# Optimization experiments

Measured on AMD Instinct MI355X. Metric: run time of the kernel, lower is better.

## Reference

```python
import jax, jax.numpy as jnp
import numpy as np

HIDDEN_DIM = 2048
PROJ_IN = 3 * 56 * 56  # 9408
PROJ_OUT = 1024
N_CLASSES = 65
BS = 2048


def setup_inputs() -> dict:
    key = jax.random.key(0)
    k1, k2, k3, k4, k5, k6 = jax.random.split(key, 6)
    z1 = jax.random.normal(k1, (BS, HIDDEN_DIM), dtype=jnp.float32)
    z2 = jax.random.normal(k2, (BS, 3, 56, 56), dtype=jnp.float32)
    # nn.Linear params: weight [out, in], bias [out]
    W_proj = jax.random.normal(k3, (PROJ_OUT, PROJ_IN), dtype=jnp.float32) * (PROJ_IN ** -0.5)
    b_proj = jax.random.normal(k4, (PROJ_OUT,), dtype=jnp.float32) * 0.01
    W_fc = jax.random.normal(k5, (N_CLASSES, HIDDEN_DIM + PROJ_OUT), dtype=jnp.float32) * ((HIDDEN_DIM + PROJ_OUT) ** -0.5)
    b_fc = jax.random.normal(k6, (N_CLASSES,), dtype=jnp.float32) * 0.01
    return {"z1": z1, "z2": z2, "W_proj": W_proj, "b_proj": b_proj, "W_fc": W_fc, "b_fc": b_fc}


def reference(z1, z2, W_proj, b_proj, W_fc, b_fc):
    bs = z1.shape[0]
    # z2 branch: flatten -> Linear -> ReLU -> detach (stop_gradient)
    z2f = z2.reshape(bs, -1)                                  # [bs, 9408]
    z2p = jax.nn.relu(z2f @ W_proj.T + b_proj)                # [bs, 1024]
    z2p = jax.lax.stop_gradient(z2p)
    # test=True path. fc_c2(cat(z1_i, z2_j)) = z1_i @ W1^T + z2_j @ W2^T + b
    # (exact split of the linear layer; same math as repeat+cat+linear).
    d1 = z1.shape[1]
    s1 = z1 @ W_fc[:, :d1].T                                  # [bs, 65]
    s2 = z2p @ W_fc[:, d1:].T                                 # [bs, 65]
    pair = s1[:, None, :] + s2[None, :, :] + b_fc             # [bs, bs, 65]
    return jnp.sum(pair, axis=1)                              # [bs, 65]
```

## Files before the change

kernel.cpp:

```cpp
#include <hip/hip_runtime.h>
#include <hip/hip_bf16.h>
#include <stdint.h>

#define BSZ   2048
#define KDIM  9408
#define NPROJ 1024
#define D1    2048
#define NCLS  65
#define NPAD  80
#define DFC   3072
#define KSTEPS 147

using bf16x8 = __attribute__((ext_vector_type(8))) short;
using f32x4  = __attribute__((ext_vector_type(4))) float;

__device__ __forceinline__ short f2bf(float f) {
    __hip_bfloat16 h = __float2bfloat16(f);
    return __builtin_bit_cast(short, h);
}

__device__ __forceinline__ void gload16(const void* g, void* l) {
    __builtin_amdgcn_global_load_lds(
        (const __attribute__((address_space(1))) void*)g,
        (__attribute__((address_space(3))) void*)l, 16, 0, 0);
}

__global__ void cvt_bf16(const float* __restrict__ src, short* __restrict__ dst, int n8)
{
    int i = blockIdx.x * blockDim.x + threadIdx.x;
    const int stride = gridDim.x * blockDim.x;
    for (; i < n8; i += stride) {
        const float4 v0 = *(const float4*)(src + (size_t)i * 8);
        const float4 v1 = *(const float4*)(src + (size_t)i * 8 + 4);
        bf16x8 s;
        s[0] = f2bf(v0.x); s[1] = f2bf(v0.y); s[2] = f2bf(v0.z); s[3] = f2bf(v0.w);
        s[4] = f2bf(v1.x); s[5] = f2bf(v1.y); s[6] = f2bf(v1.z); s[7] = f2bf(v1.w);
        *(bf16x8*)(dst + (size_t)i * 8) = s;
    }
}

__global__ void w1pad_kernel(const float* __restrict__ Wf, short* __restrict__ W1)
{
    const int chunk = blockIdx.x * 256 + threadIdx.x;
    const int row = chunk >> 8;
    const int col = (chunk & 255) * 8;
    bf16x8 s;
    if (row < NCLS) {
        const float* g = Wf + (size_t)row * DFC + col;
        float4 v0 = *(const float4*)g;
        float4 v1 = *(const float4*)(g + 4);
        s[0] = f2bf(v0.x); s[1] = f2bf(v0.y); s[2] = f2bf(v0.z); s[3] = f2bf(v0.w);
        s[4] = f2bf(v1.x); s[5] = f2bf(v1.y); s[6] = f2bf(v1.z); s[7] = f2bf(v1.w);
    } else {
        s = (bf16x8){0,0,0,0,0,0,0,0};
    }
    *(bf16x8*)(W1 + (size_t)row * D1 + col) = s;
}

template<int KS>
__global__ __launch_bounds__(256, 2)
void gemm_bf16(const short* __restrict__ A,
               const short* __restrict__ B,
               float* __restrict__ Cpart)
{
    __shared__ __align__(16) short Alds[128 * 64];
    __shared__ __align__(16) short Blds[128 * 64];

    const int t = threadIdx.x;
    const int cpx = (128 * KS) >> 3;
    int bid = blockIdx.x;
    bid = (bid & 7) * cpx + (bid >> 3);
    const int bm = bid & 15;
    const int bn = (bid >> 4) & 7;
    const int ks = bid >> 7;
    const int nsteps = KSTEPS / KS;

    const int l = t & 63, w = t >> 6;
    const int wr = w >> 1, wc = w & 1;
    const int lr = l & 15, lg = l >> 4;

    const int srow = t >> 3;
    const int scol = (t & 7) * 8;

    const short* ga = A + (size_t)(bm * 128) * KDIM;
    const short* gb = B + (size_t)(bn * 128) * KDIM;

    f32x4 acc[4][4];
#pragma unroll
    for (int m = 0; m < 4; ++m)
#pragma unroll
        for (int n = 0; n < 4; ++n)
            acc[m][n] = (f32x4){0.f, 0.f, 0.f, 0.f};

    for (int step = 0; step < nsteps; ++step) {
        const int k0 = (ks * nsteps + step) * 64;

#pragma unroll
        for (int p = 0; p < 4; ++p)
            gload16(ga + (size_t)(p * 32 + srow) * KDIM + k0 + scol,
                    (char*)Alds + p * 4096 + t * 16);
#pragma unroll
        for (int p = 0; p < 4; ++p)
            gload16(gb + (size_t)(p * 32 + srow) * KDIM + k0 + scol,
                    (char*)Blds + p * 4096 + t * 16);
        __syncthreads();

#pragma unroll
        for (int kk = 0; kk < 2; ++kk) {
            const int kb = kk * 32 + lg * 8;
            bf16x8 af[4], bfr[4];
#pragma unroll
            for (int m = 0; m < 4; ++m)
                af[m] = *(bf16x8*)&Alds[(wr * 64 + m * 16 + lr) * 64 + kb];
#pragma unroll
            for (int n = 0; n < 4; ++n)
                bfr[n] = *(bf16x8*)&Blds[(wc * 64 + n * 16 + lr) * 64 + kb];
#pragma unroll
            for (int m = 0; m < 4; ++m)
#pragma unroll
                for (int n = 0; n < 4; ++n)
                    acc[m][n] = __builtin_amdgcn_mfma_f32_16x16x32_bf16(
                        af[m], bfr[n], acc[m][n], 0, 0, 0);
        }
        __syncthreads();
    }

    float* Cp = Cpart + ((size_t)ks * BSZ + bm * 128) * NPROJ + bn * 128;
#pragma unroll
    for (int m = 0; m < 4; ++m)
#pragma unroll
        for (int r = 0; r < 4; ++r) {
            const int i = wr * 64 + m * 16 + lg * 4 + r;
#pragma unroll
            for (int n = 0; n < 4; ++n)
                Cp[(size_t)i * NPROJ + wc * 64 + n * 16 + lr] = acc[m][n][r];
        }
}

template<int KS2>
__global__ __launch_bounds__(256, 2)
void fc2_gemm(const float* __restrict__ z1,
              const short* __restrict__ W1,
              float* __restrict__ Cp2)
{
    __shared__ __align__(16) short Alds[128 * 64];
    __shared__ __align__(16) short Blds[NPAD * 64];

    const int t  = threadIdx.x;
    const int bm = blockIdx.x & 15;
    const int ks = blockIdx.x >> 4;
    const int nsteps = (D1 / 64) / KS2;

    const int l = t & 63, w = t >> 6;
    const int lr = l & 15, lg = l >> 4;
    const int srow = t >> 3;
    const int scol = (t & 7) * 8;

    f32x4 acc[2][5];
#pragma unroll
    for (int m = 0; m < 2; ++m)
#pragma unroll
        for (int n = 0; n < 5; ++n)
            acc[m][n] = (f32x4){0.f, 0.f, 0.f, 0.f};

    for (int step = 0; step < nsteps; ++step) {
        const int k0 = (ks * nsteps + step) * 64;

#pragma unroll
        for (int p = 0; p < 4; ++p) {
            const int row = p * 32 + srow;
            const float* g = z1 + (size_t)(bm * 128 + row) * D1 + k0 + scol;
            float4 v0 = *(const float4*)g;
            float4 v1 = *(const float4*)(g + 4);
            bf16x8 s;
            s[0] = f2bf(v0.x); s[1] = f2bf(v0.y); s[2] = f2bf(v0.z); s[3] = f2bf(v0.w);
            s[4] = f2bf(v1.x); s[5] = f2bf(v1.y); s[6] = f2bf(v1.z); s[7] = f2bf(v1.w);
            *(bf16x8*)&Alds[row * 64 + scol] = s;
        }
#pragma unroll
        for (int p = 0; p < 2; ++p) {
            const int chunk = p * 256 + t;
            gload16(W1 + (size_t)(chunk >> 3) * D1 + k0 + (chunk & 7) * 8,
                    (char*)Blds + chunk * 16);
        }
        if (t < 128) {
            const int chunk = 512 + t;
            gload16(W1 + (size_t)(chunk >> 3) * D1 + k0 + (chunk & 7) * 8,
                    (char*)Blds + chunk * 16);
        }
        __syncthreads();

#pragma unroll
        for (int kk = 0; kk < 2; ++kk) {
            const int kb = kk * 32 + lg * 8;
            bf16x8 af[2], bfr[5];
#pragma unroll
            for (int m = 0; m < 2; ++m)
                af[m] = *(bf16x8*)&Alds[(w * 32 + m * 16 + lr) * 64 + kb];
#pragma unroll
            for (int n = 0; n < 5; ++n)
                bfr[n] = *(bf16x8*)&Blds[(n * 16 + lr) * 64 + kb];
#pragma unroll
            for (int m = 0; m < 2; ++m)
#pragma unroll
                for (int n = 0; n < 5; ++n)
                    acc[m][n] = __builtin_amdgcn_mfma_f32_16x16x32_bf16(
                        af[m], bfr[n], acc[m][n], 0, 0, 0);
        }
        __syncthreads();
    }

    float* C = Cp2 + ((size_t)ks * BSZ + bm * 128) * NPAD;
#pragma unroll
    for (int m = 0; m < 2; ++m)
#pragma unroll
        for (int r = 0; r < 4; ++r) {
            const int i = w * 32 + m * 16 + lg * 4 + r;
#pragma unroll
            for (int n = 0; n < 5; ++n)
                C[(size_t)i * NPAD + n * 16 + lr] = acc[m][n][r];
        }
}

template<int KS2>
__global__ void reduce2_kernel(const float* __restrict__ Cp2,
                               const float* __restrict__ sconst,
                               float* __restrict__ out)
{
    const int i = blockIdx.x * 2 + (threadIdx.x >> 7);
    const int c = threadIdx.x & 127;
    if (c >= NCLS) return;
    float s = 0.f;
#pragma unroll
    for (int ksi = 0; ksi < KS2; ++ksi)
        s += Cp2[((size_t)ksi * BSZ + i) * NPAD + c];
    out[(size_t)i * NCLS + c] = 2048.0f * s + sconst[c];
}

template<int KS>
__global__ __launch_bounds__(256, 2)
void gemm_relu_f32(const float* __restrict__ A, const float* __restrict__ B,
                   const float* __restrict__ bias, float* __restrict__ Cpart,
                   float* __restrict__ colsum)
{
    __shared__ __align__(16) short Alds[128 * 64];
    __shared__ __align__(16) short Blds[128 * 64];

    const int t  = threadIdx.x;
    const int bm = blockIdx.x, bn = blockIdx.y, ks = blockIdx.z;
    const int nsteps = KSTEPS / KS;
    const int l  = t & 63, w = t >> 6;
    const int wr = w >> 1, wc = w & 1;
    const int lr = l & 15, lg = l >> 4;
    const int srow = t >> 3, scol = (t & 7) * 8;
    const int sswz = (srow & 7) * 8;
    const int rswz = (lr & 7) * 8;

    const float* ga = A + (size_t)(bm * 128 + srow) * KDIM + scol;
    const float* gb = B + (size_t)(bn * 128 + srow) * KDIM + scol;

    f32x4 acc[4][4];
#pragma unroll
    for (int m = 0; m < 4; ++m)
#pragma unroll
        for (int n = 0; n < 4; ++n)
            acc[m][n] = (f32x4){0.f, 0.f, 0.f, 0.f};

    for (int step = 0; step < nsteps; ++step) {
        const int k0 = (ks * nsteps + step) * 64;
#pragma unroll
        for (int p = 0; p < 4; ++p) {
            const float* g = ga + (size_t)(p * 32) * KDIM + k0;
            float4 v0 = *(const float4*)g;
            float4 v1 = *(const float4*)(g + 4);
            bf16x8 s;
            s[0] = f2bf(v0.x); s[1] = f2bf(v0.y); s[2] = f2bf(v0.z); s[3] = f2bf(v0.w);
            s[4] = f2bf(v1.x); s[5] = f2bf(v1.y); s[6] = f2bf(v1.z); s[7] = f2bf(v1.w);
            *(bf16x8*)&Alds[(p * 32 + srow) * 64 + (scol ^ sswz)] = s;
        }
#pragma unroll
        for (int p = 0; p < 4; ++p) {
            const float* g = gb + (size_t)(p * 32) * KDIM + k0;
            float4 v0 = *(const float4*)g;
            float4 v1 = *(const float4*)(g + 4);
            bf16x8 s;
            s[0] = f2bf(v0.x); s[1] = f2bf(v0.y); s[2] = f2bf(v0.z); s[3] = f2bf(v0.w);
            s[4] = f2bf(v1.x); s[5] = f2bf(v1.y); s[6] = f2bf(v1.z); s[7] = f2bf(v1.w);
            *(bf16x8*)&Blds[(p * 32 + srow) * 64 + (scol ^ sswz)] = s;
        }
        __syncthreads();
#pragma unroll
        for (int kk = 0; kk < 2; ++kk) {
            const int kb = (kk * 32 + lg * 8) ^ rswz;
            bf16x8 af[4], bfr[4];
#pragma unroll
            for (int m = 0; m < 4; ++m)
                af[m] = *(bf16x8*)&Alds[(wr * 64 + m * 16 + lr) * 64 + kb];
#pragma unroll
            for (int n = 0; n < 4; ++n)
                bfr[n] = *(bf16x8*)&Blds[(wc * 64 + n * 16 + lr) * 64 + kb];
#pragma unroll
            for (int m = 0; m < 4; ++m)
#pragma unroll
                for (int n = 0; n < 4; ++n)
                    acc[m][n] = __builtin_amdgcn_mfma_f32_16x16x32_bf16(
                        af[m], bfr[n], acc[m][n], 0, 0, 0);
        }
        __syncthreads();
    }

    if constexpr (KS == 1) {
        __shared__ float cls[128];
        if (t < 128) cls[t] = 0.f;
        __syncthreads();
#pragma unroll
        for (int n = 0; n < 4; ++n) {
            const int o = wc * 64 + n * 16 + lr;
            const float bv = bias[bn * 128 + o];
            float ps = 0.f;
#pragma unroll
            for (int m = 0; m < 4; ++m)
#pragma unroll
                for (int r = 0; r < 4; ++r) {
                    float v = acc[m][n][r] + bv;
                    ps += v > 0.f ? v : 0.f;
                }
            atomicAdd(&cls[o], ps);
        }
        __syncthreads();
        if (t < 128) atomicAdd(&colsum[bn * 128 + t], cls[t]);
    } else {
        float* Cp = Cpart + ((size_t)ks * BSZ + bm * 128) * NPROJ + bn * 128;
#pragma unroll
        for (int m = 0; m < 4; ++m)
#pragma unroll
            for (int r = 0; r < 4; ++r) {
                const int i = wr * 64 + m * 16 + lg * 4 + r;
#pragma unroll
                for (int n = 0; n < 4; ++n)
                    Cp[(size_t)i * NPROJ + wc * 64 + n * 16 + lr] = acc[m][n][r];
            }
    }
}

template<int KS>
__global__ void reduce_colsum(const float* __restrict__ Cpart,
                              const float* __restrict__ bias,
                              float* __restrict__ colsum)
{
    const int col = blockIdx.y * 256 + threadIdx.x;
    const int r0  = blockIdx.x * 16;
    const float bv = bias[col];
    float p = 0.f;
    for (int r = 0; r < 16; ++r) {
        float s = bv;
#pragma unroll
        for (int si = 0; si < KS; ++si)
            s += Cpart[((size_t)si * BSZ + r0 + r) * NPROJ + col];
        p += fmaxf(s, 0.f);
    }
    atomicAdd(&colsum[col], p);
}

__global__ void sconst_kernel(const float* __restrict__ colsum,
                              const float* __restrict__ Wfc,
                              const float* __restrict__ bfc,
                              float* __restrict__ sconst)
{
    const int c = blockIdx.x;
    const int l = threadIdx.x;
    const float* wr = Wfc + (size_t)c * DFC + D1;
    float p = 0.f;
#pragma unroll
    for (int j = 0; j < 16; ++j)
        p += colsum[l + j * 64] * wr[l + j * 64];
#pragma unroll
    for (int off = 32; off; off >>= 1)
        p += __shfl_xor(p, off);
    if (l == 0) sconst[c] = p + 2048.0f * bfc[c];
}

__global__ __launch_bounds__(256)
void fc1_kernel(const float* __restrict__ z1,
                const float* __restrict__ Wfc,
                const float* __restrict__ sconst,
                float* __restrict__ out)
{
    const int l = threadIdx.x & 63;
    const int w = threadIdx.x >> 6;
    const int i = blockIdx.x * 4 + w;
    const float* zr = z1 + (size_t)i * D1;
    float4 za[8];
#pragma unroll
    for (int j = 0; j < 8; ++j)
        za[j] = *(const float4*)&zr[j * 256 + l * 4];
    for (int c = 0; c < NCLS; ++c) {
        const float* wrow = Wfc + (size_t)c * DFC;
        float acc = 0.f;
#pragma unroll
        for (int j = 0; j < 8; ++j) {
            float4 wv = *(const float4*)&wrow[j * 256 + l * 4];
            acc += za[j].x * wv.x + za[j].y * wv.y + za[j].z * wv.z + za[j].w * wv.w;
        }
#pragma unroll
        for (int off = 32; off; off >>= 1)
            acc += __shfl_xor(acc, off);
        if (l == 0) out[(size_t)i * NCLS + c] = 2048.0f * acc + sconst[c];
    }
}

extern "C" void kernel_launch(void* const* d_in, const int* in_sizes, int n_in,
                              void* d_out, int out_size, void* d_ws, size_t ws_size,
                              hipStream_t stream)
{
    (void)in_sizes; (void)n_in; (void)out_size;
    const float* z1  = (const float*)d_in[0];
    const float* z2  = (const float*)d_in[1];
    const float* Wp  = (const float*)d_in[2];
    const float* bp  = (const float*)d_in[3];
    const float* Wf  = (const float*)d_in[4];
    const float* bfc = (const float*)d_in[5];
    float* out = (float*)d_out;

    float* colsum = (float*)d_ws;
    float* sconst = (float*)d_ws + 1024;
    size_t off = 8192;

    const size_t w1_sz = (size_t)NPAD * D1 * 2;
    const size_t c2_sz = (size_t)16 * BSZ * NPAD * 4;
    const bool fc2_ok = ws_size >= off + w1_sz + c2_sz;
    short* W1  = (short*)((char*)d_ws + off);
    float* Cp2 = (float*)((char*)d_ws + off + w1_sz);
    if (fc2_ok) off += w1_sz + c2_sz;

    const size_t z2bf_sz = (size_t)BSZ * KDIM * 2;
    const size_t wp_sz   = (size_t)NPROJ * KDIM * 2;
    const size_t perKS   = (size_t)BSZ * NPROJ * 4;
    const size_t rem = ws_size > off ? ws_size - off : 0;

    hipMemsetAsync(d_ws, 0, 8192, stream);

    int main_ks = 0;
    if      (rem >= z2bf_sz + wp_sz + 7 * perKS) main_ks = 7;
    else if (rem >= z2bf_sz + wp_sz + 3 * perKS) main_ks = 3;
    else if (rem >= z2bf_sz + wp_sz + 1 * perKS) main_ks = 1;

    if (main_ks > 0) {
        short* z2bf  = (short*)((char*)d_ws + off);
        short* wpbf  = (short*)((char*)d_ws + off + z2bf_sz);
        float* Cpart = (float*)((char*)d_ws + off + z2bf_sz + wp_sz);
        cvt_bf16<<<2048, 256, 0, stream>>>(z2, z2bf, BSZ * KDIM / 8);
        cvt_bf16<<<1024, 256, 0, stream>>>(Wp, wpbf, NPROJ * KDIM / 8);
        if (main_ks == 7) {
            gemm_bf16<7><<<896, 256, 0, stream>>>(z2bf, wpbf, Cpart);
            reduce_colsum<7><<<dim3(128, 4), 256, 0, stream>>>(Cpart, bp, colsum);
        } else if (main_ks == 3) {
            gemm_bf16<3><<<384, 256, 0, stream>>>(z2bf, wpbf, Cpart);
            reduce_colsum<3><<<dim3(128, 4), 256, 0, stream>>>(Cpart, bp, colsum);
        } else {
            gemm_bf16<1><<<128, 256, 0, stream>>>(z2bf, wpbf, Cpart);
            reduce_colsum<1><<<dim3(128, 4), 256, 0, stream>>>(Cpart, bp, colsum);
        }
    } else if (rem >= 7 * perKS) {
        float* Cpart = (float*)((char*)d_ws + off);
        gemm_relu_f32<7><<<dim3(16, 8, 7), 256, 0, stream>>>(z2, Wp, bp, Cpart, colsum);
        reduce_colsum<7><<<dim3(128, 4), 256, 0, stream>>>(Cpart, bp, colsum);
    } else {
        gemm_relu_f32<1><<<dim3(16, 8, 1), 256, 0, stream>>>(z2, Wp, bp,
                                                             (float*)((char*)d_ws + off), colsum);
    }

    sconst_kernel<<<65, 64, 0, stream>>>(colsum, Wf, bfc, sconst);

    if (fc2_ok) {
        w1pad_kernel<<<80, 256, 0, stream>>>(Wf, W1);
        fc2_gemm<16><<<256, 256, 0, stream>>>(z1, W1, Cp2);
        reduce2_kernel<16><<<1024, 256, 0, stream>>>(Cp2, sconst, out);
    } else {
        fc1_kernel<<<512, 256, 0, stream>>>(z1, Wf, sconst, out);
    }
}
```

Measured before the change: 249.4 us.

## Fuse conversions and memset, co-launch fc2 GEMM with projection GEMM

Merges the z2, W_proj and W_fc bf16 conversions and the workspace zeroing into one fused_cvt launch. It then runs the projection GEMM and the fc2 GEMM as separate block ranges of a single combined kernel, with launch bounds raised to 4 blocks per CU. This removes several launches and lets the small fc2 work fill idle CU slots next to the big GEMM. The higher occupancy target may squeeze registers, and the fc2 blocks compete with the main GEMM for bandwidth.

```diff
diff --git a/kernel.cpp b/kernel.cpp
--- a/kernel.cpp
+++ b/kernel.cpp
@@ -25,18 +25,252 @@
         (__attribute__((address_space(3))) void*)l, 16, 0, 0);
 }
 
+__device__ __forceinline__ bf16x8 cvt8(const float* g) {
+    float4 v0 = *(const float4*)g;
+    float4 v1 = *(const float4*)(g + 4);
+    bf16x8 s;
+    s[0] = f2bf(v0.x); s[1] = f2bf(v0.y); s[2] = f2bf(v0.z); s[3] = f2bf(v0.w);
+    s[4] = f2bf(v1.x); s[5] = f2bf(v1.y); s[6] = f2bf(v1.z); s[7] = f2bf(v1.w);
+    return s;
+}
+
+#define NC_Z2 (BSZ * KDIM / 8)
+#define NC_WP (NPROJ * KDIM / 8)
+#define NC_W1 (NPAD * D1 / 8)
+#define NC_TOT (NC_Z2 + NC_WP + NC_W1)
+
+__global__ void fused_cvt(const float* __restrict__ z2, short* __restrict__ z2bf,
+                          const float* __restrict__ Wp, short* __restrict__ wpbf,
+                          const float* __restrict__ Wf, short* __restrict__ W1,
+                          float* __restrict__ wshead)
+{
+    const int gid = blockIdx.x * blockDim.x + threadIdx.x;
+    if (gid < 2048) wshead[gid] = 0.f;
+    const int stride = gridDim.x * blockDim.x;
+    for (int i = gid; i < NC_TOT; i += stride) {
+        if (i < NC_Z2) {
+            *(bf16x8*)(z2bf + (size_t)i * 8) = cvt8(z2 + (size_t)i * 8);
+        } else if (i < NC_Z2 + NC_WP) {
+            const int j = i - NC_Z2;
+            *(bf16x8*)(wpbf + (size_t)j * 8) = cvt8(Wp + (size_t)j * 8);
+        } else {
+            const int c = i - NC_Z2 - NC_WP;
+            const int row = c >> 8;
+            const int col = (c & 255) * 8;
+            bf16x8 s = (bf16x8){0,0,0,0,0,0,0,0};
+            if (row < NCLS) s = cvt8(Wf + (size_t)row * DFC + col);
+            *(bf16x8*)(W1 + (size_t)row * D1 + col) = s;
+        }
+    }
+}
+
+template<int KS>
+__global__ __launch_bounds__(256, 4)
+void gemm_combo(const short* __restrict__ A,
+                const short* __restrict__ B,
+                float* __restrict__ Cpart,
+                const float* __restrict__ z1,
+                const short* __restrict__ W1,
+                float* __restrict__ Cp2)
+{
+    __shared__ __align__(16) char smem[32768];
+    short* Alds = (short*)smem;
+    short* Blds = (short*)(smem + 16384);
+
+    const int t = threadIdx.x;
+    const int l = t & 63, w = t >> 6;
+    const int lr = l & 15, lg = l >> 4;
+    const int srow = t >> 3;
+    const int scol = (t & 7) * 8;
+
+    if (blockIdx.x < 128 * KS) {
+        const int cpx = (128 * KS) >> 3;
+        int bid = blockIdx.x;
+        bid = (bid & 7) * cpx + (bid >> 3);
+        const int bm = bid & 15;
+        const int bn = (bid >> 4) & 7;
+        const int ks = bid >> 7;
+        const int nsteps = KSTEPS / KS;
+
+        const int wr = w >> 1, wc = w & 1;
+        const short* ga = A + (size_t)(bm * 128) * KDIM;
+        const short* gb = B + (size_t)(bn * 128) * KDIM;
+
+        f32x4 acc[4][4];
+#pragma unroll
+        for (int m = 0; m < 4; ++m)
+#pragma unroll
+            for (int n = 0; n < 4; ++n)
+                acc[m][n] = (f32x4){0.f, 0.f, 0.f, 0.f};
+
+        for (int step = 0; step < nsteps; ++step) {
+            const int k0 = (ks * nsteps + step) * 64;
+#pragma unroll
+            for (int p = 0; p < 4; ++p)
+                gload16(ga + (size_t)(p * 32 + srow) * KDIM + k0 + scol,
+                        (char*)Alds + p * 4096 + t * 16);
+#pragma unroll
+            for (int p = 0; p < 4; ++p)
+                gload16(gb + (size_t)(p * 32 + srow) * KDIM + k0 + scol,
+                        (char*)Blds + p * 4096 + t * 16);
+            __syncthreads();
+
+#pragma unroll
+            for (int kk = 0; kk < 2; ++kk) {
+                const int kb = kk * 32 + lg * 8;
+                bf16x8 af[4], bfr[4];
+#pragma unroll
+                for (int m = 0; m < 4; ++m)
+                    af[m] = *(bf16x8*)&Alds[(wr * 64 + m * 16 + lr) * 64 + kb];
+#pragma unroll
+                for (int n = 0; n < 4; ++n)
+                    bfr[n] = *(bf16x8*)&Blds[(wc * 64 + n * 16 + lr) * 64 + kb];
+#pragma unroll
+                for (int m = 0; m < 4; ++m)
+#pragma unroll
+                    for (int n = 0; n < 4; ++n)
+                        acc[m][n] = __builtin_amdgcn_mfma_f32_16x16x32_bf16(
+                            af[m], bfr[n], acc[m][n], 0, 0, 0);
+            }
+            __syncthreads();
+        }
+
+        float* Cp = Cpart + ((size_t)ks * BSZ + bm * 128) * NPROJ + bn * 128;
+#pragma unroll
+        for (int m = 0; m < 4; ++m)
+#pragma unroll
+            for (int r = 0; r < 4; ++r) {
+                const int i = wr * 64 + m * 16 + lg * 4 + r;
+#pragma unroll
+                for (int n = 0; n < 4; ++n)
+                    Cp[(size_t)i * NPROJ + wc * 64 + n * 16 + lr] = acc[m][n][r];
+            }
+    } else {
+        const int fbid = blockIdx.x - 128 * KS;
+        const int bm = fbid & 15;
+        const int ks = fbid >> 4;
+
+        f32x4 acc[2][5];
+#pragma unroll
+        for (int m = 0; m < 2; ++m)
+#pragma unroll
+            for (int n = 0; n < 5; ++n)
+                acc[m][n] = (f32x4){0.f, 0.f, 0.f, 0.f};
+
+#pragma unroll
+        for (int step = 0; step < 2; ++step) {
+            const int k0 = (ks * 2 + step) * 64;
+
+#pragma unroll
+            for (int p = 0; p < 4; ++p) {
+                const int row = p * 32 + srow;
+                *(bf16x8*)&Alds[row * 64 + scol] =
+                    cvt8(z1 + (size_t)(bm * 128 + row) * D1 + k0 + scol);
+            }
+#pragma unroll
+            for (int p = 0; p < 2; ++p) {
+                const int chunk = p * 256 + t;
+                gload16(W1 + (size_t)(chunk >> 3) * D1 + k0 + (chunk & 7) * 8,
+                        (char*)Blds + chunk * 16);
+            }
+            if (t < 128) {
+                const int chunk = 512 + t;
+                gload16(W1 + (size_t)(chunk >> 3) * D1 + k0 + (chunk & 7) * 8,
+                        (char*)Blds + chunk * 16);
+            }
+            __syncthreads();
+
+#pragma unroll
+            for (int kk = 0; kk < 2; ++kk) {
+                const int kb = kk * 32 + lg * 8;
+                bf16x8 af[2], bfr[5];
+#pragma unroll
+                for (int m = 0; m < 2; ++m)
+                    af[m] = *(bf16x8*)&Alds[(w * 32 + m * 16 + lr) * 64 + kb];
+#pragma unroll
+                for (int n = 0; n < 5; ++n)
+                    bfr[n] = *(bf16x8*)&Blds[(n * 16 + lr) * 64 + kb];
+#pragma unroll
+                for (int m = 0; m < 2; ++m)
+#pragma unroll
+                    for (int n = 0; n < 5; ++n)
+                        acc[m][n] = __builtin_amdgcn_mfma_f32_16x16x32_bf16(
+                            af[m], bfr[n], acc[m][n], 0, 0, 0);
+            }
+            __syncthreads();
+        }
+
+        float* C = Cp2 + ((size_t)ks * BSZ + bm * 128) * NPAD;
+#pragma unroll
+        for (int m = 0; m < 2; ++m)
+#pragma unroll
+            for (int r = 0; r < 4; ++r) {
+                const int i = w * 32 + m * 16 + lg * 4 + r;
+#pragma unroll
+                for (int n = 0; n < 5; ++n)
+                    C[(size_t)i * NPAD + n * 16 + lr] = acc[m][n][r];
+            }
+    }
+}
+
+template<int KS>
+__global__ void reduce_colsum(const float* __restrict__ Cpart,
+                              const float* __restrict__ bias,
+                              float* __restrict__ colsum)
+{
+    const int col = blockIdx.y * 256 + threadIdx.x;
+    const int r0  = blockIdx.x * 16;
+    const float bv = bias[col];
+    float p = 0.f;
+    for (int r = 0; r < 16; ++r) {
+        float s = bv;
+#pragma unroll
+        for (int si = 0; si < KS; ++si)
+            s += Cpart[((size_t)si * BSZ + r0 + r) * NPROJ + col];
+        p += fmaxf(s, 0.f);
+    }
+    atomicAdd(&colsum[col], p);
+}
+
+__global__ void sconst_kernel(const float* __restrict__ colsum,
+                              const float* __restrict__ Wfc,
+                              const float* __restrict__ bfc,
+                              float* __restrict__ sconst)
+{
+    const int c = blockIdx.x;
+    const int l = threadIdx.x;
+    const float* wr = Wfc + (size_t)c * DFC + D1;
+    float p = 0.f;
+#pragma unroll
+    for (int j = 0; j < 16; ++j)
+        p += colsum[l + j * 64] * wr[l + j * 64];
+#pragma unroll
+    for (int off = 32; off; off >>= 1)
+        p += __shfl_xor(p, off);
+    if (l == 0) sconst[c] = p + 2048.0f * bfc[c];
+}
+
+template<int KS2>
+__global__ void reduce2_kernel(const float* __restrict__ Cp2,
+                               const float* __restrict__ sconst,
+                               float* __restrict__ out)
+{
+    const int i = blockIdx.x * 2 + (threadIdx.x >> 7);
+    const int c = threadIdx.x & 127;
+    if (c >= NCLS) return;
+    float s = 0.f;
+#pragma unroll
+    for (int ksi = 0; ksi < KS2; ++ksi)
+        s += Cp2[((size_t)ksi * BSZ + i) * NPAD + c];
+    out[(size_t)i * NCLS + c] = 2048.0f * s + sconst[c];
+}
+
 __global__ void cvt_bf16(const float* __restrict__ src, short* __restrict__ dst, int n8)
 {
     int i = blockIdx.x * blockDim.x + threadIdx.x;
     const int stride = gridDim.x * blockDim.x;
-    for (; i < n8; i += stride) {
-        const float4 v0 = *(const float4*)(src + (size_t)i * 8);
-        const float4 v1 = *(const float4*)(src + (size_t)i * 8 + 4);
-        bf16x8 s;
-        s[0] = f2bf(v0.x); s[1] = f2bf(v0.y); s[2] = f2bf(v0.z); s[3] = f2bf(v0.w);
-        s[4] = f2bf(v1.x); s[5] = f2bf(v1.y); s[6] = f2bf(v1.z); s[7] = f2bf(v1.w);
-        *(bf16x8*)(dst + (size_t)i * 8) = s;
-    }
+    for (; i < n8; i += stride)
+        *(bf16x8*)(dst + (size_t)i * 8) = cvt8(src + (size_t)i * 8);
 }
 
 __global__ void w1pad_kernel(const float* __restrict__ Wf, short* __restrict__ W1)
@@ -44,28 +278,18 @@
     const int chunk = blockIdx.x * 256 + threadIdx.x;
     const int row = chunk >> 8;
     const int col = (chunk & 255) * 8;
-    bf16x8 s;
-    if (row < NCLS) {
-        const float* g = Wf + (size_t)row * DFC + col;
-        float4 v0 = *(const float4*)g;
-        float4 v1 = *(const float4*)(g + 4);
-        s[0] = f2bf(v0.x); s[1] = f2bf(v0.y); s[2] = f2bf(v0.z); s[3] = f2bf(v0.w);
-        s[4] = f2bf(v1.x); s[5] = f2bf(v1.y); s[6] = f2bf(v1.z); s[7] = f2bf(v1.w);
-    } else {
-        s = (bf16x8){0,0,0,0,0,0,0,0};
-    }
+    bf16x8 s = (bf16x8){0,0,0,0,0,0,0,0};
+    if (row < NCLS) s = cvt8(Wf + (size_t)row * DFC + col);
     *(bf16x8*)(W1 + (size_t)row * D1 + col) = s;
 }
 
 template<int KS>
 __global__ __launch_bounds__(256, 2)
-void gemm_bf16(const short* __restrict__ A,
-               const short* __restrict__ B,
+void gemm_bf16(const short* __restrict__ A, const short* __restrict__ B,
                float* __restrict__ Cpart)
 {
     __shared__ __align__(16) short Alds[128 * 64];
     __shared__ __align__(16) short Blds[128 * 64];
-
     const int t = threadIdx.x;
     const int cpx = (128 * KS) >> 3;
     int bid = blockIdx.x;
@@ -74,27 +298,19 @@
     const int bn = (bid >> 4) & 7;
     const int ks = bid >> 7;
     const int nsteps = KSTEPS / KS;
-
     const int l = t & 63, w = t >> 6;
     const int wr = w >> 1, wc = w & 1;
     const int lr = l & 15, lg = l >> 4;
-
-    const int srow = t >> 3;
-    const int scol = (t & 7) * 8;
-
+    const int srow = t >> 3, scol = (t & 7) * 8;
     const short* ga = A + (size_t)(bm * 128) * KDIM;
     const short* gb = B + (size_t)(bn * 128) * KDIM;
-
     f32x4 acc[4][4];
 #pragma unroll
     for (int m = 0; m < 4; ++m)
 #pragma unroll
-        for (int n = 0; n < 4; ++n)
-            acc[m][n] = (f32x4){0.f, 0.f, 0.f, 0.f};
-
+        for (int n = 0; n < 4; ++n) acc[m][n] = (f32x4){0.f,0.f,0.f,0.f};
     for (int step = 0; step < nsteps; ++step) {
         const int k0 = (ks * nsteps + step) * 64;
-
 #pragma unroll
         for (int p = 0; p < 4; ++p)
             gload16(ga + (size_t)(p * 32 + srow) * KDIM + k0 + scol,
@@ -104,7 +320,6 @@
             gload16(gb + (size_t)(p * 32 + srow) * KDIM + k0 + scol,
                     (char*)Blds + p * 4096 + t * 16);
         __syncthreads();
-
 #pragma unroll
         for (int kk = 0; kk < 2; ++kk) {
             const int kb = kk * 32 + lg * 8;
@@ -124,7 +339,6 @@
         }
         __syncthreads();
     }
-
     float* Cp = Cpart + ((size_t)ks * BSZ + bm * 128) * NPROJ + bn * 128;
 #pragma unroll
     for (int m = 0; m < 4; ++m)
@@ -139,43 +353,30 @@
 
 template<int KS2>
 __global__ __launch_bounds__(256, 2)
-void fc2_gemm(const float* __restrict__ z1,
-              const short* __restrict__ W1,
+void fc2_gemm(const float* __restrict__ z1, const short* __restrict__ W1,
               float* __restrict__ Cp2)
 {
     __shared__ __align__(16) short Alds[128 * 64];
     __shared__ __align__(16) short Blds[NPAD * 64];
-
     const int t  = threadIdx.x;
     const int bm = blockIdx.x & 15;
     const int ks = blockIdx.x >> 4;
     const int nsteps = (D1 / 64) / KS2;
-
     const int l = t & 63, w = t >> 6;
     const int lr = l & 15, lg = l >> 4;
-    const int srow = t >> 3;
-    const int scol = (t & 7) * 8;
-
+    const int srow = t >> 3, scol = (t & 7) * 8;
     f32x4 acc[2][5];
 #pragma unroll
     for (int m = 0; m < 2; ++m)
 #pragma unroll
-        for (int n = 0; n < 5; ++n)
-            acc[m][n] = (f32x4){0.f, 0.f, 0.f, 0.f};
-
+        for (int n = 0; n < 5; ++n) acc[m][n] = (f32x4){0.f,0.f,0.f,0.f};
     for (int step = 0; step < nsteps; ++step) {
         const int k0 = (ks * nsteps + step) * 64;
-
 #pragma unroll
         for (int p = 0; p < 4; ++p) {
             const int row = p * 32 + srow;
-            const float* g = z1 + (size_t)(bm * 128 + row) * D1 + k0 + scol;
-            float4 v0 = *(const float4*)g;
-            float4 v1 = *(const float4*)(g + 4);
-            bf16x8 s;
-            s[0] = f2bf(v0.x); s[1] = f2bf(v0.y); s[2] = f2bf(v0.z); s[3] = f2bf(v0.w);
-            s[4] = f2bf(v1.x); s[5] = f2bf(v1.y); s[6] = f2bf(v1.z); s[7] = f2bf(v1.w);
-            *(bf16x8*)&Alds[row * 64 + scol] = s;
+            *(bf16x8*)&Alds[row * 64 + scol] =
+                cvt8(z1 + (size_t)(bm * 128 + row) * D1 + k0 + scol);
         }
 #pragma unroll
         for (int p = 0; p < 2; ++p) {
@@ -189,7 +390,6 @@
                     (char*)Blds + chunk * 16);
         }
         __syncthreads();
-
 #pragma unroll
         for (int kk = 0; kk < 2; ++kk) {
             const int kb = kk * 32 + lg * 8;
@@ -209,7 +409,6 @@
         }
         __syncthreads();
     }
-
     float* C = Cp2 + ((size_t)ks * BSZ + bm * 128) * NPAD;
 #pragma unroll
     for (int m = 0; m < 2; ++m)
@@ -220,21 +419,6 @@
             for (int n = 0; n < 5; ++n)
                 C[(size_t)i * NPAD + n * 16 + lr] = acc[m][n][r];
         }
-}
-
-template<int KS2>
-__global__ void reduce2_kernel(const float* __restrict__ Cp2,
-                               const float* __restrict__ sconst,
-                               float* __restrict__ out)
-{
-    const int i = blockIdx.x * 2 + (threadIdx.x >> 7);
-    const int c = threadIdx.x & 127;
-    if (c >= NCLS) return;
-    float s = 0.f;
-#pragma unroll
-    for (int ksi = 0; ksi < KS2; ++ksi)
-        s += Cp2[((size_t)ksi * BSZ + i) * NPAD + c];
-    out[(size_t)i * NCLS + c] = 2048.0f * s + sconst[c];
 }
 
 template<int KS>
@@ -245,7 +429,6 @@
 {
     __shared__ __align__(16) short Alds[128 * 64];
     __shared__ __align__(16) short Blds[128 * 64];
-
     const int t  = threadIdx.x;
     const int bm = blockIdx.x, bn = blockIdx.y, ks = blockIdx.z;
     const int nsteps = KSTEPS / KS;
@@ -255,39 +438,23 @@
     const int srow = t >> 3, scol = (t & 7) * 8;
     const int sswz = (srow & 7) * 8;
     const int rswz = (lr & 7) * 8;
-
     const float* ga = A + (size_t)(bm * 128 + srow) * KDIM + scol;
     const float* gb = B + (size_t)(bn * 128 + srow) * KDIM + scol;
-
     f32x4 acc[4][4];
 #pragma unroll
     for (int m = 0; m < 4; ++m)
 #pragma unroll
-        for (int n = 0; n < 4; ++n)
-            acc[m][n] = (f32x4){0.f, 0.f, 0.f, 0.f};
-
+        for (int n = 0; n < 4; ++n) acc[m][n] = (f32x4){0.f,0.f,0.f,0.f};
     for (int step = 0; step < nsteps; ++step) {
         const int k0 = (ks * nsteps + step) * 64;
 #pragma unroll
-        for (int p = 0; p < 4; ++p) {
-            const float* g = ga + (size_t)(p * 32) * KDIM + k0;
-            float4 v0 = *(const float4*)g;
-            float4 v1 = *(const float4*)(g + 4);
-            bf16x8 s;
-            s[0] = f2bf(v0.x); s[1] = f2bf(v0.y); s[2] = f2bf(v0.z); s[3] = f2bf(v0.w);
-            s[4] = f2bf(v1.x); s[5] = f2bf(v1.y); s[6] = f2bf(v1.z); s[7] = f2bf(v1.w);
-            *(bf16x8*)&Alds[(p * 32 + srow) * 64 + (scol ^ sswz)] = s;
-        }
-#pragma unroll
-        for (int p = 0; p < 4; ++p) {
-            const float* g = gb + (size_t)(p * 32) * KDIM + k0;
-            float4 v0 = *(const float4*)g;
-            float4 v1 = *(const float4*)(g + 4);
-            bf16x8 s;
-            s[0] = f2bf(v0.x); s[1] = f2bf(v0.y); s[2] = f2bf(v0.z); s[3] = f2bf(v0.w);
-            s[4] = f2bf(v1.x); s[5] = f2bf(v1.y); s[6] = f2bf(v1.z); s[7] = f2bf(v1.w);
-            *(bf16x8*)&Blds[(p * 32 + srow) * 64 + (scol ^ sswz)] = s;
-        }
+        for (int p = 0; p < 4; ++p)
+            *(bf16x8*)&Alds[(p * 32 + srow) * 64 + (scol ^ sswz)] =
+                cvt8(ga + (size_t)(p * 32) * KDIM + k0);
+#pragma unroll
+        for (int p = 0; p < 4; ++p)
+            *(bf16x8*)&Blds[(p * 32 + srow) * 64 + (scol ^ sswz)] =
+                cvt8(gb + (size_t)(p * 32) * KDIM + k0);
         __syncthreads();
 #pragma unroll
         for (int kk = 0; kk < 2; ++kk) {
@@ -308,7 +475,6 @@
         }
         __syncthreads();
     }
-
     if constexpr (KS == 1) {
         __shared__ float cls[128];
         if (t < 128) cls[t] = 0.f;
@@ -343,48 +509,9 @@
     }
 }
 
-template<int KS>
-__global__ void reduce_colsum(const float* __restrict__ Cpart,
-                              const float* __restrict__ bias,
-                              float* __restrict__ colsum)
-{
-    const int col = blockIdx.y * 256 + threadIdx.x;
-    const int r0  = blockIdx.x * 16;
-    const float bv = bias[col];
-    float p = 0.f;
-    for (int r = 0; r < 16; ++r) {
-        float s = bv;
-#pragma unroll
-        for (int si = 0; si < KS; ++si)
-            s += Cpart[((size_t)si * BSZ + r0 + r) * NPROJ + col];
-        p += fmaxf(s, 0.f);
-    }
-    atomicAdd(&colsum[col], p);
-}
-
-__global__ void sconst_kernel(const float* __restrict__ colsum,
-                              const float* __restrict__ Wfc,
-                              const float* __restrict__ bfc,
-                              float* __restrict__ sconst)
-{
-    const int c = blockIdx.x;
-    const int l = threadIdx.x;
-    const float* wr = Wfc + (size_t)c * DFC + D1;
-    float p = 0.f;
-#pragma unroll
-    for (int j = 0; j < 16; ++j)
-        p += colsum[l + j * 64] * wr[l + j * 64];
-#pragma unroll
-    for (int off = 32; off; off >>= 1)
-        p += __shfl_xor(p, off);
-    if (l == 0) sconst[c] = p + 2048.0f * bfc[c];
-}
-
 __global__ __launch_bounds__(256)
-void fc1_kernel(const float* __restrict__ z1,
-                const float* __restrict__ Wfc,
-                const float* __restrict__ sconst,
-                float* __restrict__ out)
+void fc1_kernel(const float* __restrict__ z1, const float* __restrict__ Wfc,
+                const float* __restrict__ sconst, float* __restrict__ out)
 {
     const int l = threadIdx.x & 63;
     const int w = threadIdx.x >> 6;
@@ -426,23 +553,39 @@
     float* sconst = (float*)d_ws + 1024;
     size_t off = 8192;
 
-    const size_t w1_sz = (size_t)NPAD * D1 * 2;
-    const size_t c2_sz = (size_t)16 * BSZ * NPAD * 4;
+    const size_t w1_sz   = (size_t)NPAD * D1 * 2;
+    const size_t c2_sz   = (size_t)16 * BSZ * NPAD * 4;
+    const size_t z2bf_sz = (size_t)BSZ * KDIM * 2;
+    const size_t wp_sz   = (size_t)NPROJ * KDIM * 2;
+    const size_t perKS   = (size_t)BSZ * NPROJ * 4;
+
+    const size_t needA = off + w1_sz + c2_sz + z2bf_sz + wp_sz + 7 * perKS;
+
+    if (ws_size >= needA) {
+        short* W1    = (short*)((char*)d_ws + off);
+        float* Cp2   = (float*)((char*)d_ws + off + w1_sz);
+        short* z2bf  = (short*)((char*)d_ws + off + w1_sz + c2_sz);
+        short* wpbf  = (short*)((char*)d_ws + off + w1_sz + c2_sz + z2bf_sz);
+        float* Cpart = (float*)((char*)d_ws + off + w1_sz + c2_sz + z2bf_sz + wp_sz);
+
+        fused_cvt<<<2048, 256, 0, stream>>>(z2, z2bf, Wp, wpbf, Wf, W1, (float*)d_ws);
+        gemm_combo<7><<<896 + 256, 256, 0, stream>>>(z2bf, wpbf, Cpart, z1, W1, Cp2);
+        reduce_colsum<7><<<dim3(128, 4), 256, 0, stream>>>(Cpart, bp, colsum);
+        sconst_kernel<<<65, 64, 0, stream>>>(colsum, Wf, bfc, sconst);
+        reduce2_kernel<16><<<1024, 256, 0, stream>>>(Cp2, sconst, out);
+        return;
+    }
+
+    hipMemsetAsync(d_ws, 0, 8192, stream);
+
     const bool fc2_ok = ws_size >= off + w1_sz + c2_sz;
     short* W1  = (short*)((char*)d_ws + off);
     float* Cp2 = (float*)((char*)d_ws + off + w1_sz);
     if (fc2_ok) off += w1_sz + c2_sz;
-
-    const size_t z2bf_sz = (size_t)BSZ * KDIM * 2;
-    const size_t wp_sz   = (size_t)NPROJ * KDIM * 2;
-    const size_t perKS   = (size_t)BSZ * NPROJ * 4;
     const size_t rem = ws_size > off ? ws_size - off : 0;
 
-    hipMemsetAsync(d_ws, 0, 8192, stream);
-
     int main_ks = 0;
-    if      (rem >= z2bf_sz + wp_sz + 7 * perKS) main_ks = 7;
-    else if (rem >= z2bf_sz + wp_sz + 3 * perKS) main_ks = 3;
+    if      (rem >= z2bf_sz + wp_sz + 3 * perKS) main_ks = 3;
     else if (rem >= z2bf_sz + wp_sz + 1 * perKS) main_ks = 1;
 
     if (main_ks > 0) {
@@ -451,10 +594,7 @@
         float* Cpart = (float*)((char*)d_ws + off + z2bf_sz + wp_sz);
         cvt_bf16<<<2048, 256, 0, stream>>>(z2, z2bf, BSZ * KDIM / 8);
         cvt_bf16<<<1024, 256, 0, stream>>>(Wp, wpbf, NPROJ * KDIM / 8);
-        if (main_ks == 7) {
-            gemm_bf16<7><<<896, 256, 0, stream>>>(z2bf, wpbf, Cpart);
-            reduce_colsum<7><<<dim3(128, 4), 256, 0, stream>>>(Cpart, bp, colsum);
-        } else if (main_ks == 3) {
+        if (main_ks == 3) {
             gemm_bf16<3><<<384, 256, 0, stream>>>(z2bf, wpbf, Cpart);
             reduce_colsum<3><<<dim3(128, 4), 256, 0, stream>>>(Cpart, bp, colsum);
         } else {
```

New measurement: 234.3 us. 6.1% less time.
